# Kernel optimization log

Measured on AMD Instinct MI355X. Metric: run time of the kernel, lower is better.

The kernel has to match this reference:

```python
import jax, jax.numpy as jnp
import numpy as np

N, L, S, D, H = 2, 2048, 2048, 128, 32  # batch, query len, state len, hidden_dim(=head dim), num_heads


def setup_inputs() -> dict:
    key = jax.random.key(0)
    ks = jax.random.split(key, 8)
    return {
        "query": jax.random.normal(ks[0], (N, L, D), dtype=jnp.float32),
        "states": jax.random.normal(ks[1], (N, S, D), dtype=jnp.float32),
        "Wk": jax.random.normal(ks[2], (H, D, D), dtype=jnp.float32) * 0.05,
        "bk": jax.random.normal(ks[3], (H, D), dtype=jnp.float32) * 0.05,
        "Wv": jax.random.normal(ks[4], (H, D, D), dtype=jnp.float32) * 0.05,
        "bv": jax.random.normal(ks[5], (H, D), dtype=jnp.float32) * 0.05,
        "Wc": jax.random.normal(ks[6], (H * D, D), dtype=jnp.float32) * 0.02,
        "bc": jax.random.normal(ks[7], (D,), dtype=jnp.float32) * 0.02,
    }


def reference(query, states, Wk, bk, Wv, bv, Wc, bc):
    # Per-head key/value projections (Attention.keys_mlp / values_mlp), batched over heads.
    K = jnp.einsum('nsd,hdk->nhsk', states, Wk) + bk[None, :, None, :]  # [N,H,S,D]
    V = jnp.einsum('nsd,hdk->nhsk', states, Wv) + bv[None, :, None, :]  # [N,H,S,D]
    scale = jnp.sqrt(jnp.asarray(K.shape[-1], query.dtype))
    logits = jnp.einsum('nld,nhsd->nhls', query, K) / scale            # [N,H,L,S]
    # Original detaches attention scores (softmax(...).detach()).
    A = jax.lax.stop_gradient(jax.nn.softmax(logits, axis=-1))
    ctx = jnp.einsum('nhls,nhsd->nhld', A, V)                          # [N,H,L,D]
    n, h, l, d = ctx.shape
    ctx = ctx.transpose(0, 2, 1, 3).reshape(n, l, h * d)               # concat heads -> [N,L,H*D]
    return ctx @ Wc + bc                                               # context_transform
```

## Files before the change

### kernel.cpp

```cpp
#include <hip/hip_runtime.h>
#include <hip/hip_bf16.h>

#define N_B 2
#define L_Q 2048
#define S_S 2048
#define D_D 128
#define H_H 32
#define SCALEK (0.08838834764831845f * 1.4426950408889634f)

typedef __attribute__((ext_vector_type(8))) short bf8;
typedef __attribute__((ext_vector_type(4))) short bf4;
typedef __attribute__((ext_vector_type(4))) float f4;

#define MFMA(a, b, c) __builtin_amdgcn_mfma_f32_16x16x32_bf16(a, b, c, 0, 0, 0)

__device__ __forceinline__ short f2bf(float x) {
    union { float f; unsigned u; } v; v.f = x;
    unsigned r = v.u + 0x7FFFu + ((v.u >> 16) & 1u);
    return (short)(r >> 16);
}

__device__ __forceinline__ bf4 pk4(float a, float b, float c, float d) {
    union { __hip_bfloat162 h2[2]; bf4 v; } u;
    u.h2[0] = __float22bfloat162_rn(make_float2(a, b));
    u.h2[1] = __float22bfloat162_rn(make_float2(c, d));
    return u.v;
}

__device__ __forceinline__ bf8 cat44(bf4 lo, bf4 hi) {
    bf8 r;
    r[0] = lo[0]; r[1] = lo[1]; r[2] = lo[2]; r[3] = lo[3];
    r[4] = hi[0]; r[5] = hi[1]; r[6] = hi[2]; r[7] = hi[3];
    return r;
}

__device__ __forceinline__ bf8 load8(const float* p) {
    const float4* q = (const float4*)p;
    float4 a = q[0], b = q[1];
    bf8 r;
    r[0] = f2bf(a.x); r[1] = f2bf(a.y); r[2] = f2bf(a.z); r[3] = f2bf(a.w);
    r[4] = f2bf(b.x); r[5] = f2bf(b.y); r[6] = f2bf(b.z); r[7] = f2bf(b.w);
    return r;
}

__device__ __forceinline__ void async16(const void* g, void* l) {
    __builtin_amdgcn_global_load_lds(
        (const __attribute__((address_space(1))) unsigned*)g,
        (__attribute__((address_space(3))) unsigned*)l, 16, 0, 0);
}

__global__ __launch_bounds__(256) void k_wct(const float* __restrict__ Wc,
                                             unsigned short* __restrict__ WcF) {
    int f16 = blockIdx.x * 256 + threadIdx.x;
    int l = f16 & 63, t = (f16 >> 6) & 3, nfA = (f16 >> 8) & 7, kc = f16 >> 11;
    int lrow = l & 15, lgrp = l >> 4;
    int kbase = kc * 128 + t * 32 + lgrp * 8;
    int n = nfA * 16 + lrow;
    bf8 v;
    #pragma unroll
    for (int j = 0; j < 8; ++j) v[j] = f2bf(Wc[(size_t)(kbase + j) * D_D + n]);
    *(bf8*)(WcF + (size_t)f16 * 8) = v;
}

__global__ __launch_bounds__(256) void k_wt(const float* __restrict__ Wk,
        const float* __restrict__ Wv, unsigned short* __restrict__ WkF,
        unsigned short* __restrict__ WvF) {
    __shared__ unsigned short T[128][129];
    const int tid = threadIdx.x;
    const int h = blockIdx.x;
    const int job = blockIdx.y;
    const float* W = (job ? Wv : Wk) + (size_t)h * (D_D * D_D);
    unsigned short* WF = (job ? WvF : WkF) + (size_t)h * (D_D * D_D);

    #pragma unroll
    for (int i = 0; i < 64; ++i) {
        int flat = i * 256 + tid;
        T[flat >> 7][flat & 127] = (unsigned short)f2bf(W[flat]);
    }
    __syncthreads();
    #pragma unroll
    for (int j8 = 0; j8 < 8; ++j8) {
        int f16 = j8 * 256 + tid;
        int l = f16 & 63, t = (f16 >> 6) & 3, df = (f16 >> 8) & 7;
        int lrow = l & 15, lgrp = l >> 4;
        bf8 v;
        #pragma unroll
        for (int j = 0; j < 8; ++j) v[j] = (short)T[t * 32 + lgrp * 8 + j][df * 16 + lrow];
        *(bf8*)(WF + (size_t)f16 * 8) = v;
    }
}

__global__ __launch_bounds__(256) void k_proj(const float* __restrict__ states,
        const unsigned short* __restrict__ WkF, const float* __restrict__ bk,
        const unsigned short* __restrict__ WvF, const float* __restrict__ bv,
        unsigned short* __restrict__ Kb, unsigned short* __restrict__ VTb) {
    const int tid = threadIdx.x;
    const int l = tid & 63, w = tid >> 6;
    const int lrow = l & 15, lgrp = l >> 4;
    const int bx = blockIdx.x;
    const int sc = bx & 31;
    const int nh = bx >> 5;
    const int h = nh & 31, n = nh >> 5;
    const int job = blockIdx.y;

    if (job == 0) {
        const unsigned short* WF = WkF + (size_t)h * (D_D * D_D);
        const float* srow = states + ((size_t)n * S_S + sc * 64 + w * 16 + lrow) * D_D;
        bf8 a[4];
        #pragma unroll
        for (int t = 0; t < 4; ++t) a[t] = load8(srow + t * 32 + lgrp * 8);
        f4 acc[8];
        #pragma unroll
        for (int i = 0; i < 8; ++i) acc[i] = (f4)(0.f);
        #pragma unroll
        for (int nf = 0; nf < 8; ++nf) {
            #pragma unroll
            for (int t = 0; t < 4; ++t) {
                bf8 b = *(const bf8*)(WF + (((nf * 4 + t) * 64 + l) << 3));
                acc[nf] = MFMA(a[t], b, acc[nf]);
            }
        }
        unsigned short* Kout = Kb + (size_t)(n * H_H + h) * S_S * D_D;
        #pragma unroll
        for (int nf = 0; nf < 8; ++nf) {
            int dcol = nf * 16 + lrow;
            float bias = bk[h * D_D + dcol];
            #pragma unroll
            for (int r = 0; r < 4; ++r) {
                int srw = sc * 64 + w * 16 + lgrp * 4 + r;
                Kout[(size_t)srw * D_D + dcol] = (unsigned short)f2bf((acc[nf][r] + bias) * SCALEK);
            }
        }
    } else {
        const unsigned short* WF = WvF + (size_t)h * (D_D * D_D);
        bf8 a[2][4];
        #pragma unroll
        for (int mf = 0; mf < 2; ++mf) {
            #pragma unroll
            for (int t = 0; t < 4; ++t)
                a[mf][t] = *(const bf8*)(WF + ((((w * 2 + mf) * 4 + t) * 64 + l) << 3));
        }
        f4 acc[2][4];
        #pragma unroll
        for (int mf = 0; mf < 2; ++mf)
            #pragma unroll
            for (int nf = 0; nf < 4; ++nf) acc[mf][nf] = (f4)(0.f);
        #pragma unroll
        for (int nf = 0; nf < 4; ++nf) {
            const float* srow = states + ((size_t)n * S_S + sc * 64 + nf * 16 + lrow) * D_D;
            #pragma unroll
            for (int t = 0; t < 4; ++t) {
                bf8 b = load8(srow + t * 32 + lgrp * 8);
                acc[0][nf] = MFMA(a[0][t], b, acc[0][nf]);
                acc[1][nf] = MFMA(a[1][t], b, acc[1][nf]);
            }
        }
        unsigned short* Vout = VTb + (size_t)(n * H_H + h) * D_D * S_S;
        #pragma unroll
        for (int mf = 0; mf < 2; ++mf) {
            #pragma unroll
            for (int r = 0; r < 4; ++r) {
                int drow = w * 32 + mf * 16 + lgrp * 4 + r;
                float bias = bv[h * D_D + drow];
                #pragma unroll
                for (int nf = 0; nf < 4; ++nf) {
                    int p = ((nf >> 1) << 5) + ((lrow >> 2) << 3) + ((nf & 1) << 2) + (lrow & 3);
                    int scol = sc * 64 + p;
                    Vout[(size_t)drow * S_S + scol] = (unsigned short)f2bf(acc[mf][nf][r] + bias);
                }
            }
        }
    }
}

__global__ __launch_bounds__(256, 3) void k_attn(const float* __restrict__ query,
        const unsigned short* __restrict__ Kb, const unsigned short* __restrict__ VTb,
        unsigned short* __restrict__ CTX) {
    __shared__ char smem[32768];
    const int tid = threadIdx.x;
    const int l = tid & 63, w = tid >> 6;
    const int lrow = l & 15, lgrp = l >> 4;

    const int bid = blockIdx.x;
    const int bx = (bid & 7) * 128 + (bid >> 3);
    const int qt = bx & 15;
    const int nh = bx >> 4;
    const int h = nh & 31, n = nh >> 5;
    const int qbase = qt * 128 + w * 32;

    bf8 qf[2][4];
    #pragma unroll
    for (int mf = 0; mf < 2; ++mf) {
        const float* qp = query + ((size_t)n * L_Q + qbase + mf * 16 + lrow) * D_D;
        #pragma unroll
        for (int t = 0; t < 4; ++t) qf[mf][t] = load8(qp + t * 32 + lgrp * 8);
    }

    f4 oacc[2][8];
    #pragma unroll
    for (int mf = 0; mf < 2; ++mf)
        #pragma unroll
        for (int df = 0; df < 8; ++df) oacc[mf][df] = (f4)(0.f);
    float rsum[2] = {0.f, 0.f};

    const char* Kg = (const char*)(Kb + (size_t)(n * H_H + h) * S_S * D_D);
    const char* Vg = (const char*)(VTb + (size_t)(n * H_H + h) * D_D * S_S);

    auto stage = [&](int c, int sc2) {
        char* Kl = smem + c * 8192;
        char* Vl = smem + 16384 + c * 8192;
        #pragma unroll
        for (int i = 0; i < 2; ++i) {
            int kop = w * 2 + i;
            int o = kop * 1024 + l * 16;
            int r = o >> 8;
            int b = (o & 255) ^ ((r & 7) << 4);
            async16(Kg + (size_t)(sc2 * 32 + r) * 256 + b, Kl + kop * 1024);
        }
        #pragma unroll
        for (int i = 0; i < 2; ++i) {
            int vop = w * 2 + i;
            int o = vop * 1024 + l * 16;
            int drow = o >> 6;
            int b = (o & 63) ^ (((drow >> 1) & 3) << 4);
            async16(Vg + (size_t)drow * 4096 + sc2 * 64 + b, Vl + vop * 1024);
        }
    };

    auto iter = [&](int cur, int sc2, bool prefetch) {
        if (prefetch) stage(cur ^ 1, sc2 + 1);
        const char* Klds = smem + cur * 8192;
        const char* Vlds = smem + 16384 + cur * 8192;

        f4 sacc[2][2];
        #pragma unroll
        for (int mf = 0; mf < 2; ++mf)
            #pragma unroll
            for (int nf = 0; nf < 2; ++nf) sacc[mf][nf] = (f4)(0.f);
        __builtin_amdgcn_s_setprio(1);
        #pragma unroll
        for (int nf = 0; nf < 2; ++nf) {
            int srow = nf * 16 + lrow;
            int swz = (srow & 7) << 4;
            #pragma unroll
            for (int t = 0; t < 4; ++t) {
                bf8 kb = *(const bf8*)(Klds + srow * 256 + (((t * 32 + lgrp * 8) * 2) ^ swz));
                sacc[0][nf] = MFMA(kb, qf[0][t], sacc[0][nf]);
                sacc[1][nf] = MFMA(kb, qf[1][t], sacc[1][nf]);
            }
        }
        __builtin_amdgcn_s_setprio(0);

        bf8 pf[2];
        #pragma unroll
        for (int mf = 0; mf < 2; ++mf) {
            bf4 pblk[2];
            #pragma unroll
            for (int nf = 0; nf < 2; ++nf) {
                float p0 = __builtin_amdgcn_exp2f(sacc[mf][nf][0]);
                float p1 = __builtin_amdgcn_exp2f(sacc[mf][nf][1]);
                float p2 = __builtin_amdgcn_exp2f(sacc[mf][nf][2]);
                float p3 = __builtin_amdgcn_exp2f(sacc[mf][nf][3]);
                rsum[mf] += (p0 + p1) + (p2 + p3);
                pblk[nf] = pk4(p0, p1, p2, p3);
            }
            pf[mf] = cat44(pblk[0], pblk[1]);
        }

        __builtin_amdgcn_s_setprio(1);
        #pragma unroll
        for (int df = 0; df < 8; ++df) {
            int drow = df * 16 + lrow;
            bf8 vf = *(const bf8*)(Vlds + drow * 64 + ((lgrp * 16) ^ (((drow >> 1) & 3) << 4)));
            oacc[0][df] = MFMA(vf, pf[0], oacc[0][df]);
            oacc[1][df] = MFMA(vf, pf[1], oacc[1][df]);
        }
        __builtin_amdgcn_s_setprio(0);
        __syncthreads();
    };

    stage(0, 0);
    __syncthreads();
    for (int s2 = 0; s2 < 64; s2 += 2) {
        iter(0, s2, true);
        iter(1, s2 + 1, s2 + 1 < 63);
    }

    float rinv[2];
    #pragma unroll
    for (int mf = 0; mf < 2; ++mf) {
        float v = rsum[mf];
        v += __shfl_xor(v, 16, 64);
        v += __shfl_xor(v, 32, 64);
        rinv[mf] = 1.f / v;
    }
    #pragma unroll
    for (int mf = 0; mf < 2; ++mf) {
        int qrow = qbase + mf * 16 + lrow;
        unsigned short* crow = CTX + (size_t)(n * L_Q + qrow) * 4096 + h * D_D;
        #pragma unroll
        for (int df = 0; df < 8; ++df) {
            bf4 o = pk4(oacc[mf][df][0] * rinv[mf], oacc[mf][df][1] * rinv[mf],
                        oacc[mf][df][2] * rinv[mf], oacc[mf][df][3] * rinv[mf]);
            *(bf4*)(crow + df * 16 + lgrp * 4) = o;
        }
    }
}

__global__ __launch_bounds__(256) void k_out(const unsigned short* __restrict__ CTX,
        const unsigned short* __restrict__ WcF, const float* __restrict__ bc,
        float* __restrict__ out) {
    __shared__ char Alds[8192];
    const int tid = threadIdx.x;
    const int l = tid & 63, w = tid >> 6;
    const int lrow = l & 15, lgrp = l >> 4;
    const int m0 = blockIdx.x * 16;
    const char* Ag = (const char*)(CTX + (size_t)m0 * 4096);

    auto stage = [&](int c, int kc) {
        int o = w * 1024 + l * 16;
        int r = o >> 8;
        int b = (o & 255) ^ ((r & 7) << 4);
        async16(Ag + (size_t)r * 8192 + kc * 256 + b, Alds + c * 4096 + w * 1024);
    };

    f4 acc[2];
    acc[0] = (f4)(0.f); acc[1] = (f4)(0.f);
    stage(0, 0);
    __syncthreads();
    int cur = 0;
    for (int kc = 0; kc < 32; ++kc) {
        if (kc < 31) stage(cur ^ 1, kc + 1);
        const char* Ac = Alds + cur * 4096;
        #pragma unroll
        for (int t = 0; t < 4; ++t) {
            int swz = (lrow & 7) << 4;
            bf8 a = *(const bf8*)(Ac + lrow * 256 + (((t * 32 + lgrp * 8) * 2) ^ swz));
            #pragma unroll
            for (int nf = 0; nf < 2; ++nf) {
                int nfA = w * 2 + nf;
                bf8 b = *(const bf8*)(WcF + ((size_t)(((kc * 8 + nfA) * 4 + t) * 64 + l) << 3));
                acc[nf] = MFMA(a, b, acc[nf]);
            }
        }
        __syncthreads();
        cur ^= 1;
    }
    #pragma unroll
    for (int nf = 0; nf < 2; ++nf) {
        int nc = w * 32 + nf * 16 + lrow;
        float bias = bc[nc];
        #pragma unroll
        for (int r = 0; r < 4; ++r)
            out[(size_t)(m0 + lgrp * 4 + r) * D_D + nc] = acc[nf][r] + bias;
    }
}

extern "C" void kernel_launch(void* const* d_in, const int* in_sizes, int n_in,
                              void* d_out, int out_size, void* d_ws, size_t ws_size,
                              hipStream_t stream) {
    const float* query  = (const float*)d_in[0];
    const float* states = (const float*)d_in[1];
    const float* Wk = (const float*)d_in[2];
    const float* bk = (const float*)d_in[3];
    const float* Wv = (const float*)d_in[4];
    const float* bv = (const float*)d_in[5];
    const float* Wc = (const float*)d_in[6];
    const float* bc = (const float*)d_in[7];
    float* out = (float*)d_out;

    char* ws = (char*)d_ws;
    unsigned short* Kb  = (unsigned short*)(ws);
    unsigned short* VTb = (unsigned short*)(ws + 33554432);
    unsigned short* CTX = (unsigned short*)(ws + 67108864);
    unsigned short* WkF = (unsigned short*)(ws + 67108864);
    unsigned short* WvF = (unsigned short*)(ws + 67108864 + 1048576);
    unsigned short* WcF = (unsigned short*)(ws + 100663296);

    k_wct<<<256, 256, 0, stream>>>(Wc, WcF);
    dim3 gw(32, 2);
    k_wt<<<gw, 256, 0, stream>>>(Wk, Wv, WkF, WvF);
    dim3 gb(2048, 2);
    k_proj<<<gb, 256, 0, stream>>>(states, WkF, bk, WvF, bv, Kb, VTb);
    k_attn<<<1024, 256, 0, stream>>>(query, Kb, VTb, CTX);
    k_out<<<256, 256, 0, stream>>>(CTX, WcF, bc, out);
}
```

Measured before the change: 232.3 us.

## Fuse K/V projection blocks and load V fragments directly from global in attention

The projection kernel now computes both K and V in one block, reusing a single load of the states tile, and writes vectorised bf4 outputs instead of scalar stores. The attention kernel drops LDS staging for V and instead loads V fragments straight from global memory into registers each iteration, halving shared memory use. Occupancy hint is lowered from 3 to 2 blocks. This aims to cut redundant state loads and LDS traffic, but the direct V loads are not prefetched and may expose global latency in the attention inner loop.

```diff
diff --git a/kernel.cpp b/kernel.cpp
--- a/kernel.cpp
+++ b/kernel.cpp
@@ -101,14 +101,38 @@
     const int sc = bx & 31;
     const int nh = bx >> 5;
     const int h = nh & 31, n = nh >> 5;
-    const int job = blockIdx.y;
-
-    if (job == 0) {
+
+    const float* srow = states + ((size_t)n * S_S + sc * 64 + w * 16 + lrow) * D_D;
+    bf8 sf[4];
+    #pragma unroll
+    for (int t = 0; t < 4; ++t) sf[t] = load8(srow + t * 32 + lgrp * 8);
+
+    {
         const unsigned short* WF = WkF + (size_t)h * (D_D * D_D);
-        const float* srow = states + ((size_t)n * S_S + sc * 64 + w * 16 + lrow) * D_D;
-        bf8 a[4];
-        #pragma unroll
-        for (int t = 0; t < 4; ++t) a[t] = load8(srow + t * 32 + lgrp * 8);
+        f4 acc[8];
+        #pragma unroll
+        for (int i = 0; i < 8; ++i) acc[i] = (f4)(0.f);
+        #pragma unroll
+        for (int mf = 0; mf < 8; ++mf) {
+            #pragma unroll
+            for (int t = 0; t < 4; ++t) {
+                bf8 a = *(const bf8*)(WF + (((mf * 4 + t) * 64 + l) << 3));
+                acc[mf] = MFMA(a, sf[t], acc[mf]);
+            }
+        }
+        unsigned short* Kout = Kb + (size_t)(n * H_H + h) * S_S * D_D
+                                  + (size_t)(sc * 64 + w * 16 + lrow) * D_D;
+        #pragma unroll
+        for (int mf = 0; mf < 8; ++mf) {
+            int d0 = mf * 16 + lgrp * 4;
+            float4 bb = *(const float4*)(bk + h * D_D + d0);
+            bf4 kv = pk4((acc[mf][0] + bb.x) * SCALEK, (acc[mf][1] + bb.y) * SCALEK,
+                         (acc[mf][2] + bb.z) * SCALEK, (acc[mf][3] + bb.w) * SCALEK);
+            *(bf4*)(Kout + d0) = kv;
+        }
+    }
+    {
+        const unsigned short* WF = WvF + (size_t)h * (D_D * D_D);
         f4 acc[8];
         #pragma unroll
         for (int i = 0; i < 8; ++i) acc[i] = (f4)(0.f);
@@ -117,66 +141,26 @@
             #pragma unroll
             for (int t = 0; t < 4; ++t) {
                 bf8 b = *(const bf8*)(WF + (((nf * 4 + t) * 64 + l) << 3));
-                acc[nf] = MFMA(a[t], b, acc[nf]);
-            }
-        }
-        unsigned short* Kout = Kb + (size_t)(n * H_H + h) * S_S * D_D;
+                acc[nf] = MFMA(sf[t], b, acc[nf]);
+            }
+        }
+        unsigned short* Vout = VTb + (size_t)(n * H_H + h) * D_D * S_S;
+        const int p0 = ((w >> 1) << 5) + (lgrp << 3) + ((w & 1) << 2);
         #pragma unroll
         for (int nf = 0; nf < 8; ++nf) {
-            int dcol = nf * 16 + lrow;
-            float bias = bk[h * D_D + dcol];
-            #pragma unroll
-            for (int r = 0; r < 4; ++r) {
-                int srw = sc * 64 + w * 16 + lgrp * 4 + r;
-                Kout[(size_t)srw * D_D + dcol] = (unsigned short)f2bf((acc[nf][r] + bias) * SCALEK);
-            }
-        }
-    } else {
-        const unsigned short* WF = WvF + (size_t)h * (D_D * D_D);
-        bf8 a[2][4];
-        #pragma unroll
-        for (int mf = 0; mf < 2; ++mf) {
-            #pragma unroll
-            for (int t = 0; t < 4; ++t)
-                a[mf][t] = *(const bf8*)(WF + ((((w * 2 + mf) * 4 + t) * 64 + l) << 3));
-        }
-        f4 acc[2][4];
-        #pragma unroll
-        for (int mf = 0; mf < 2; ++mf)
-            #pragma unroll
-            for (int nf = 0; nf < 4; ++nf) acc[mf][nf] = (f4)(0.f);
-        #pragma unroll
-        for (int nf = 0; nf < 4; ++nf) {
-            const float* srow = states + ((size_t)n * S_S + sc * 64 + nf * 16 + lrow) * D_D;
-            #pragma unroll
-            for (int t = 0; t < 4; ++t) {
-                bf8 b = load8(srow + t * 32 + lgrp * 8);
-                acc[0][nf] = MFMA(a[0][t], b, acc[0][nf]);
-                acc[1][nf] = MFMA(a[1][t], b, acc[1][nf]);
-            }
-        }
-        unsigned short* Vout = VTb + (size_t)(n * H_H + h) * D_D * S_S;
-        #pragma unroll
-        for (int mf = 0; mf < 2; ++mf) {
-            #pragma unroll
-            for (int r = 0; r < 4; ++r) {
-                int drow = w * 32 + mf * 16 + lgrp * 4 + r;
-                float bias = bv[h * D_D + drow];
-                #pragma unroll
-                for (int nf = 0; nf < 4; ++nf) {
-                    int p = ((nf >> 1) << 5) + ((lrow >> 2) << 3) + ((nf & 1) << 2) + (lrow & 3);
-                    int scol = sc * 64 + p;
-                    Vout[(size_t)drow * S_S + scol] = (unsigned short)f2bf(acc[mf][nf][r] + bias);
-                }
-            }
-        }
-    }
-}
-
-__global__ __launch_bounds__(256, 3) void k_attn(const float* __restrict__ query,
+            int d = nf * 16 + lrow;
+            float bias = bv[h * D_D + d];
+            bf4 vv = pk4(acc[nf][0] + bias, acc[nf][1] + bias,
+                         acc[nf][2] + bias, acc[nf][3] + bias);
+            *(bf4*)(Vout + (size_t)d * S_S + sc * 64 + p0) = vv;
+        }
+    }
+}
+
+__global__ __launch_bounds__(256, 2) void k_attn(const float* __restrict__ query,
         const unsigned short* __restrict__ Kb, const unsigned short* __restrict__ VTb,
         unsigned short* __restrict__ CTX) {
-    __shared__ char smem[32768];
+    __shared__ char smem[16384];
     const int tid = threadIdx.x;
     const int l = tid & 63, w = tid >> 6;
     const int lrow = l & 15, lgrp = l >> 4;
@@ -204,11 +188,10 @@
     float rsum[2] = {0.f, 0.f};
 
     const char* Kg = (const char*)(Kb + (size_t)(n * H_H + h) * S_S * D_D);
-    const char* Vg = (const char*)(VTb + (size_t)(n * H_H + h) * D_D * S_S);
+    const unsigned short* Vg = VTb + (size_t)(n * H_H + h) * D_D * S_S;
 
     auto stage = [&](int c, int sc2) {
         char* Kl = smem + c * 8192;
-        char* Vl = smem + 16384 + c * 8192;
         #pragma unroll
         for (int i = 0; i < 2; ++i) {
             int kop = w * 2 + i;
@@ -217,20 +200,15 @@
             int b = (o & 255) ^ ((r & 7) << 4);
             async16(Kg + (size_t)(sc2 * 32 + r) * 256 + b, Kl + kop * 1024);
         }
-        #pragma unroll
-        for (int i = 0; i < 2; ++i) {
-            int vop = w * 2 + i;
-            int o = vop * 1024 + l * 16;
-            int drow = o >> 6;
-            int b = (o & 63) ^ (((drow >> 1) & 3) << 4);
-            async16(Vg + (size_t)drow * 4096 + sc2 * 64 + b, Vl + vop * 1024);
-        }
     };
 
     auto iter = [&](int cur, int sc2, bool prefetch) {
+        bf8 vf[8];
+        #pragma unroll
+        for (int df = 0; df < 8; ++df)
+            vf[df] = *(const bf8*)(Vg + (size_t)(df * 16 + lrow) * S_S + sc2 * 32 + lgrp * 8);
         if (prefetch) stage(cur ^ 1, sc2 + 1);
         const char* Klds = smem + cur * 8192;
-        const char* Vlds = smem + 16384 + cur * 8192;
 
         f4 sacc[2][2];
         #pragma unroll
@@ -270,10 +248,8 @@
         __builtin_amdgcn_s_setprio(1);
         #pragma unroll
         for (int df = 0; df < 8; ++df) {
-            int drow = df * 16 + lrow;
-            bf8 vf = *(const bf8*)(Vlds + drow * 64 + ((lgrp * 16) ^ (((drow >> 1) & 3) << 4)));
-            oacc[0][df] = MFMA(vf, pf[0], oacc[0][df]);
-            oacc[1][df] = MFMA(vf, pf[1], oacc[1][df]);
+            oacc[0][df] = MFMA(vf[df], pf[0], oacc[0][df]);
+            oacc[1][df] = MFMA(vf[df], pf[1], oacc[1][df]);
         }
         __builtin_amdgcn_s_setprio(0);
         __syncthreads();
@@ -380,8 +356,7 @@
     k_wct<<<256, 256, 0, stream>>>(Wc, WcF);
     dim3 gw(32, 2);
     k_wt<<<gw, 256, 0, stream>>>(Wk, Wv, WkF, WvF);
-    dim3 gb(2048, 2);
-    k_proj<<<gb, 256, 0, stream>>>(states, WkF, bk, WvF, bv, Kb, VTb);
+    k_proj<<<2048, 256, 0, stream>>>(states, WkF, bk, WvF, bv, Kb, VTb);
     k_attn<<<1024, 256, 0, stream>>>(query, Kb, VTb, CTX);
     k_out<<<256, 256, 0, stream>>>(CTX, WcF, bc, out);
 }
```

New measurement: 348.1 us. 1.5x slower.
